# Performance work log

Measured on AMD Instinct MI355X. Metric: run time of the kernel, lower is better.

## Reference

```python
import jax, jax.numpy as jnp
import numpy as np

NUM_HEADS = 16
D_MODEL = 1024
MASK_VALUE = -1000000.0


def setup_inputs() -> dict:
    key = jax.random.key(0)
    ks = jax.random.split(key, 8)
    B, S, D = 2, 2048, D_MODEL
    scale = 1.0 / np.sqrt(D)
    return {
        "queries": jax.random.normal(ks[0], (B, S, D), dtype=jnp.float32),
        "keys": jax.random.normal(ks[1], (B, S, D), dtype=jnp.float32),
        "values": jax.random.normal(ks[2], (B, S, D), dtype=jnp.float32),
        "valid_lens": jax.random.randint(ks[3], (B,), 1, S + 1),
        # Linear weights stored as (in, out); no bias (bias=False)
        "Wq": jax.random.normal(ks[4], (D, D), dtype=jnp.float32) * scale,
        "Wk": jax.random.normal(ks[5], (D, D), dtype=jnp.float32) * scale,
        "Wv": jax.random.normal(ks[6], (D, D), dtype=jnp.float32) * scale,
        "Wo": jax.random.normal(ks[7], (D, D), dtype=jnp.float32) * scale,
    }


def reference(queries, keys, values, valid_lens, Wq, Wk, Wv, Wo):
    B, Sq, D = queries.shape
    Sk = keys.shape[1]
    H = NUM_HEADS
    hd = D // H

    def split_heads(x, S):
        # (B, S, D) -> (B, H, S, hd)
        return x.reshape(B, S, H, hd).transpose(0, 2, 1, 3)

    q = split_heads(queries @ Wq, Sq)
    k = split_heads(keys @ Wk, Sk)
    v = split_heads(values @ Wv, Sk)

    # Faithful to original bug: d_k = queries.size(0) after head-flattening = B*H
    scale = 1.0 / jnp.sqrt(jnp.float32(B * H))
    scores = jnp.einsum("bhqd,bhkd->bhqk", q, k) * scale  # (B,H,Sq,Sk)

    # sequence_mask over last dim, per batch row (valid_lens repeated per head)
    mask = jnp.arange(Sk)[None, None, None, :] < valid_lens[:, None, None, None]
    scores = jnp.where(mask, scores, MASK_VALUE)
    attn = jax.nn.softmax(scores, axis=-1)

    out = jnp.einsum("bhqk,bhkd->bhqd", attn, v)  # (B,H,Sq,hd)
    out = out.transpose(0, 2, 1, 3).reshape(B, Sq, D)
    return out @ Wo
```

## Files before the change

kernel.cpp:

```cpp
#include <hip/hip_runtime.h>
#include <stdint.h>

#define NH 16
#define SEQ 2048
#define DMODEL 1024
#define HD 64
#define NBATCH 2
#define MTOT (NBATCH * SEQ)
#define QSCALE 0.17677669529663687f
#define LOG2E 1.4426950408889634f

typedef __bf16 bf16x8 __attribute__((ext_vector_type(8)));
typedef float f32x4 __attribute__((ext_vector_type(4)));
typedef float f32x16 __attribute__((ext_vector_type(16)));
typedef unsigned uint4v __attribute__((ext_vector_type(4)));

__device__ __forceinline__ unsigned short bf16u(float x) {
  unsigned u = __builtin_bit_cast(unsigned, x);
  u += 0x7fffu + ((u >> 16) & 1u);
  return (unsigned short)(u >> 16);
}

__device__ __forceinline__ float exp2_fast(float x) {
  float r;
  asm("v_exp_f32 %0, %1" : "=v"(r) : "v"(x));
  return r;
}

__device__ __forceinline__ f32x4 mfma16(bf16x8 a, bf16x8 b, f32x4 c) {
  return __builtin_amdgcn_mfma_f32_16x16x32_bf16(a, b, c, 0, 0, 0);
}
__device__ __forceinline__ f32x16 mfma32(bf16x8 a, bf16x8 b, f32x16 c) {
  return __builtin_amdgcn_mfma_f32_32x32x16_bf16(a, b, c, 0, 0, 0);
}

__device__ __forceinline__ void gl16(const void* g, void* l) {
  __builtin_amdgcn_global_load_lds(
      (const __attribute__((address_space(1))) void*)g,
      (__attribute__((address_space(3))) void*)l, 16, 0, 0);
}

__device__ __forceinline__ unsigned cvtpk(float a, float b) {
  unsigned r;
  asm("v_cvt_pk_bf16_f32 %0, %1, %2" : "=v"(r) : "v"(a), "v"(b));
  return r;
}


__global__ __launch_bounds__(256) void prep_kernel(
    const float* __restrict__ x0, const float* __restrict__ x1,
    const float* __restrict__ x2, unsigned short* __restrict__ o0,
    unsigned short* __restrict__ o1, unsigned short* __restrict__ o2,
    const float* __restrict__ w0, const float* __restrict__ w1,
    const float* __restrict__ w2, const float* __restrict__ w3,
    unsigned short* __restrict__ t0, unsigned short* __restrict__ t1,
    unsigned short* __restrict__ t2, unsigned short* __restrict__ t3) {
  const int id = blockIdx.x;
  if (id < 1536) {
    const int src = id >> 9, blk = id & 511;
    const float* s = (src == 0) ? x0 : (src == 1) ? x1 : x2;
    unsigned short* d = (src == 0) ? o0 : (src == 1) ? o1 : o2;
    const int n4 = MTOT * DMODEL / 4;
    for (int i = blk * 256 + threadIdx.x; i < n4; i += 512 * 256) {
      float4 f = reinterpret_cast<const float4*>(s)[i];
      ushort4 u;
      u.x = bf16u(f.x); u.y = bf16u(f.y); u.z = bf16u(f.z); u.w = bf16u(f.w);
      reinterpret_cast<ushort4*>(d)[i] = u;
    }
  } else {
    __shared__ float tile[64][65];
    const int id2 = id - 1536;
    const int wsel = id2 >> 8, tl = id2 & 255;
    const float* w = (wsel == 0) ? w0 : (wsel == 1) ? w1
                     : (wsel == 2) ? w2 : w3;
    unsigned short* t = (wsel == 0) ? t0 : (wsel == 1) ? t1
                        : (wsel == 2) ? t2 : t3;
    const float scl = (wsel == 0) ? QSCALE * LOG2E : 1.0f;
    int n0 = (tl & 15) * 64, k0 = (tl >> 4) * 64;
    int tx = threadIdx.x & 63, ty = threadIdx.x >> 6;
#pragma unroll
    for (int i = 0; i < 16; ++i) {
      int kk = ty * 16 + i;
      tile[kk][tx] = w[(k0 + kk) * DMODEL + n0 + tx];
    }
    __syncthreads();
#pragma unroll
    for (int i = 0; i < 16; ++i) {
      int nn = ty * 16 + i;
      t[(n0 + nn) * DMODEL + k0 + tx] = bf16u(tile[tx][nn] * scl);
    }
  }
}

__global__ __launch_bounds__(256) void gemm_qkv_kernel(
    const unsigned short* __restrict__ xq, const unsigned short* __restrict__ xk,
    const unsigned short* __restrict__ xv,
    const unsigned short* __restrict__ wq, const unsigned short* __restrict__ wk,
    const unsigned short* __restrict__ wv,
    unsigned short* __restrict__ qb, unsigned short* __restrict__ kb,
    unsigned short* __restrict__ vb) {
  __shared__ unsigned short lA[2][128 * 32];
  __shared__ unsigned short lB[2][128 * 32];
  const int z = blockIdx.z;
  const unsigned short* A = (z == 0) ? xq : (z == 1) ? xk : xv;
  const unsigned short* Wt = (z == 0) ? wq : (z == 1) ? wk : wv;
  unsigned short* outb = (z == 0) ? qb : (z == 1) ? kb : vb;

  const int tid = threadIdx.x;
  const int lane = tid & 63, wid = tid >> 6;
  const int wr = wid >> 1, wc = wid & 1;
  const int m0 = blockIdx.x * 128, n0 = blockIdx.y * 128;
  const int lm = lane & 15, lg = lane >> 4;
  const int lk = lg * 8;

  auto stage = [&](int buf, int kt) {
#pragma unroll
    for (int i = 0; i < 2; ++i) {
      int c = tid + i * 256;
      int row = c >> 2, cb = c & 3;
      gl16(A + (m0 + row) * DMODEL + kt * 32 + cb * 8, (char*)lA[buf] + c * 16);
      gl16(Wt + (n0 + row) * DMODEL + kt * 32 + cb * 8, (char*)lB[buf] + c * 16);
    }
  };

  f32x4 acc[4][4] = {};
  stage(0, 0);
  __syncthreads();
  int cur = 0;

  for (int kt = 0; kt < DMODEL / 32; ++kt) {
    if (kt + 1 < DMODEL / 32) stage(cur ^ 1, kt + 1);

    bf16x8 af[4], bfr[4];
#pragma unroll
    for (int x = 0; x < 4; ++x) {
      af[x] = *reinterpret_cast<const bf16x8*>(&lA[cur][(wr * 64 + x * 16 + lm) * 32 + lk]);
      bfr[x] = *reinterpret_cast<const bf16x8*>(&lB[cur][(wc * 64 + x * 16 + lm) * 32 + lk]);
    }
#pragma unroll
    for (int mi = 0; mi < 4; ++mi)
#pragma unroll
      for (int ni = 0; ni < 4; ++ni)
        acc[mi][ni] = mfma16(af[mi], bfr[ni], acc[mi][ni]);

    if (kt + 1 < DMODEL / 32) { __syncthreads(); cur ^= 1; }
  }

#pragma unroll
  for (int mi = 0; mi < 4; ++mi)
#pragma unroll
    for (int ni = 0; ni < 4; ++ni) {
      int col = n0 + wc * 64 + ni * 16 + lm;
#pragma unroll
      for (int r = 0; r < 4; ++r) {
        int row = m0 + wr * 64 + mi * 16 + lg * 4 + r;
        int b = row >> 11, s = row & (SEQ - 1);
        int h = col >> 6, d = col & (HD - 1);
        outb[(((b * NH + h) * SEQ + s) * HD + d)] = bf16u(acc[mi][ni][r]);
      }
    }
}

__global__ __launch_bounds__(256) void gemm_out_kernel(
    const unsigned short* __restrict__ A, const unsigned short* __restrict__ Wt,
    float* __restrict__ outf) {
  __shared__ unsigned short lA[2][128 * 32];
  __shared__ unsigned short lB[2][64 * 32];
  const int tid = threadIdx.x;
  const int lane = tid & 63, wr = tid >> 6;
  const int m0 = blockIdx.x * 128, n0 = blockIdx.y * 64;
  const int lm = lane & 15, lg = lane >> 4;
  const int lk = lg * 8;

  auto stage = [&](int buf, int kt) {
#pragma unroll
    for (int i = 0; i < 2; ++i) {
      int c = tid + i * 256;
      int row = c >> 2, cb = c & 3;
      gl16(A + (m0 + row) * DMODEL + kt * 32 + cb * 8, (char*)lA[buf] + c * 16);
    }
    int c = tid;
    int row = c >> 2, cb = c & 3;
    gl16(Wt + (n0 + row) * DMODEL + kt * 32 + cb * 8, (char*)lB[buf] + c * 16);
  };

  f32x4 acc[2][4] = {};
  stage(0, 0);
  __syncthreads();
  int cur = 0;

  for (int kt = 0; kt < DMODEL / 32; ++kt) {
    if (kt + 1 < DMODEL / 32) stage(cur ^ 1, kt + 1);

    bf16x8 af[2], bfr[4];
#pragma unroll
    for (int x = 0; x < 2; ++x)
      af[x] = *reinterpret_cast<const bf16x8*>(&lA[cur][(wr * 32 + x * 16 + lm) * 32 + lk]);
#pragma unroll
    for (int x = 0; x < 4; ++x)
      bfr[x] = *reinterpret_cast<const bf16x8*>(&lB[cur][(x * 16 + lm) * 32 + lk]);
#pragma unroll
    for (int mi = 0; mi < 2; ++mi)
#pragma unroll
      for (int ni = 0; ni < 4; ++ni)
        acc[mi][ni] = mfma16(af[mi], bfr[ni], acc[mi][ni]);

    if (kt + 1 < DMODEL / 32) { __syncthreads(); cur ^= 1; }
  }

#pragma unroll
  for (int mi = 0; mi < 2; ++mi)
#pragma unroll
    for (int ni = 0; ni < 4; ++ni) {
      int col = n0 + ni * 16 + lm;
#pragma unroll
      for (int r = 0; r < 4; ++r) {
        int row = m0 + wr * 32 + mi * 16 + lg * 4 + r;
        outf[row * DMODEL + col] = acc[mi][ni][r];
      }
    }
}

__global__ __launch_bounds__(256) void attn16_kernel(
    const unsigned short* __restrict__ qb, const unsigned short* __restrict__ kb,
    const unsigned short* __restrict__ vb, const int* __restrict__ vlens,
    unsigned short* __restrict__ ao) {
  __shared__ char klds[4][2][8192];
  const int lane = threadIdx.x & 63;
  const int w = threadIdx.x >> 6;
  const int qi = lane & 31, hi = lane >> 5;
  const int wid = blockIdx.x * 4 + w;
  const int bhi = wid & 31;
  const int chunk = wid >> 5;
  const int b = bhi & 1, h = bhi >> 1;
  const int bh = b * NH + h;
  const int s0w = chunk * 32;
  const int vlen = vlens[b];
  const int nkt = (vlen + 63) >> 6;

  const unsigned short* kbase = kb + bh * SEQ * HD;
  const unsigned short* vbase = vb + (size_t)bh * SEQ * HD;

  const unsigned short* qrow = qb + (bh * SEQ + s0w + qi) * HD;
  bf16x8 qf[4];
#pragma unroll
  for (int ks = 0; ks < 4; ++ks)
    qf[ks] = *reinterpret_cast<const bf16x8*>(qrow + ks * 16 + hi * 8);

  f32x16 oacc[2] = {};
  float m = -3e38f, l = 0.f;

  const int srow = lane >> 3;
  const int scol8 = (lane & 7) ^ (srow & 7);
  auto stageK = [&](int buf, int kt) {
    int k0 = kt * 64;
    char* dst = &klds[w][buf][0];
#pragma unroll
    for (int i = 0; i < 8; ++i)
      gl16(kbase + (size_t)(k0 + i * 8 + srow) * HD + scol8 * 8,
           dst + i * 1024);
  };

  auto readK = [&](bf16x8* kr, int buf) {
    const char* base = &klds[w][buf][0];
#pragma unroll
    for (int kb2 = 0; kb2 < 2; ++kb2)
#pragma unroll
      for (int ks = 0; ks < 4; ++ks) {
        int row = kb2 * 32 + qi;
        int off = row * 128 + ((ks * 32 + hi * 16) ^ ((qi & 7) << 4));
        kr[kb2 * 4 + ks] = *reinterpret_cast<const bf16x8*>(base + off);
      }
  };

  auto body = [&](int t, int buf) {
    const int k0 = t * 64;
    const bool lastt = (t == nkt - 1);

    asm volatile("s_waitcnt vmcnt(0)" ::: "memory");
    __builtin_amdgcn_sched_barrier(0);

    bf16x8 kr[8];
    readK(kr, buf);

    f32x16 s0 = {}, s1 = {};
    __builtin_amdgcn_s_setprio(1);
#pragma unroll
    for (int ks = 0; ks < 4; ++ks) s0 = mfma32(kr[ks], qf[ks], s0);
#pragma unroll
    for (int ks = 0; ks < 4; ++ks) s1 = mfma32(kr[4 + ks], qf[ks], s1);
    __builtin_amdgcn_s_setprio(0);

    bf16x8 vr[8];
#pragma unroll
    for (int db = 0; db < 2; ++db)
#pragma unroll
      for (int f = 0; f < 4; ++f) {
        const unsigned short* vp =
            vbase + (size_t)(k0 + f * 16 + 4 * hi) * HD + db * 32 + qi;
        bf16x8 tv;
#pragma unroll
        for (int j = 0; j < 8; ++j) {
          int koff = ((j & 3) + 8 * (j >> 2)) * HD;
          tv[j] = *reinterpret_cast<const __bf16*>(vp + koff);
        }
        vr[db * 4 + f] = tv;
      }

    if (!lastt) stageK(buf ^ 1, t + 1);

    if (lastt) {
#pragma unroll
      for (int r = 0; r < 16; ++r) {
        int key = k0 + (r & 3) + 8 * (r >> 2) + 4 * hi;
        if (key >= vlen) s0[r] = -1.4426950e6f;
        if (key + 32 >= vlen) s1[r] = -1.4426950e6f;
      }
    }

    float mx8[8];
#pragma unroll
    for (int i = 0; i < 8; ++i)
      mx8[i] = fmaxf(fmaxf(s0[i], s0[i + 8]), fmaxf(s1[i], s1[i + 8]));
#pragma unroll
    for (int st = 4; st; st >>= 1)
#pragma unroll
      for (int i = 0; i < st; ++i) mx8[i] = fmaxf(mx8[i], mx8[i + st]);
    float mx = fmaxf(mx8[0], __shfl_xor(mx8[0], 32, 64));
    float mn = fmaxf(m, mx);
    float sf = exp2_fast(m - mn);
    m = mn;

#pragma unroll
    for (int r = 0; r < 16; ++r) s0[r] = exp2_fast(s0[r] - mn);
#pragma unroll
    for (int r = 0; r < 16; ++r) s1[r] = exp2_fast(s1[r] - mn);
    float sm8[8];
#pragma unroll
    for (int i = 0; i < 8; ++i)
      sm8[i] = (s0[i] + s0[i + 8]) + (s1[i] + s1[i + 8]);
#pragma unroll
    for (int st = 4; st; st >>= 1)
#pragma unroll
      for (int i = 0; i < st; ++i) sm8[i] += sm8[i + st];
    float ps = sm8[0] + __shfl_xor(sm8[0], 32, 64);
    l = l * sf + ps;
#pragma unroll
    for (int db = 0; db < 2; ++db) oacc[db] *= sf;

    bf16x8 pf[4];
    auto packP = [&](const f32x16& s, bf16x8* out) {
#pragma unroll
      for (int f = 0; f < 2; ++f) {
        uint4v wv;
#pragma unroll
        for (int k2 = 0; k2 < 4; ++k2)
          wv[k2] = cvtpk(s[f * 8 + k2 * 2], s[f * 8 + k2 * 2 + 1]);
        out[f] = __builtin_bit_cast(bf16x8, wv);
      }
    };
    packP(s0, pf);
    packP(s1, pf + 2);

    __builtin_amdgcn_s_setprio(1);
#pragma unroll
    for (int db = 0; db < 2; ++db)
#pragma unroll
      for (int f = 0; f < 4; ++f)
        oacc[db] = mfma32(vr[db * 4 + f], pf[f], oacc[db]);
    __builtin_amdgcn_s_setprio(0);
  };

  stageK(0, 0);
  for (int t = 0; t < nkt; ++t) body(t, t & 1);

  const float linv = 1.0f / l;
#pragma unroll
  for (int db = 0; db < 2; ++db)
#pragma unroll
    for (int rq = 0; rq < 4; ++rq) {
      ushort4 o;
      o.x = bf16u(oacc[db][rq * 4 + 0] * linv);
      o.y = bf16u(oacc[db][rq * 4 + 1] * linv);
      o.z = bf16u(oacc[db][rq * 4 + 2] * linv);
      o.w = bf16u(oacc[db][rq * 4 + 3] * linv);
      int d = db * 32 + 8 * rq + 4 * hi;
      *reinterpret_cast<ushort4*>(
          ao + (b * SEQ + s0w + qi) * DMODEL + h * HD + d) = o;
    }
}

extern "C" void kernel_launch(void* const* d_in, const int* in_sizes, int n_in,
                              void* d_out, int out_size, void* d_ws, size_t ws_size,
                              hipStream_t stream) {
  (void)in_sizes; (void)n_in; (void)out_size; (void)ws_size;
  const float* q = (const float*)d_in[0];
  const float* k = (const float*)d_in[1];
  const float* v = (const float*)d_in[2];
  const int* vlens = (const int*)d_in[3];
  const float* Wq = (const float*)d_in[4];
  const float* Wk = (const float*)d_in[5];
  const float* Wv = (const float*)d_in[6];
  const float* Wo = (const float*)d_in[7];
  float* out = (float*)d_out;

  char* ws = (char*)d_ws;
  const size_t MB = 1u << 20;
  unsigned short* xq = (unsigned short*)(ws + 0 * MB);
  unsigned short* xk = (unsigned short*)(ws + 8 * MB);
  unsigned short* xv = (unsigned short*)(ws + 16 * MB);
  unsigned short* wqt = (unsigned short*)(ws + 24 * MB);
  unsigned short* wkt = (unsigned short*)(ws + 26 * MB);
  unsigned short* wvt = (unsigned short*)(ws + 28 * MB);
  unsigned short* wot = (unsigned short*)(ws + 30 * MB);
  unsigned short* qb = (unsigned short*)(ws + 32 * MB);
  unsigned short* kb = (unsigned short*)(ws + 40 * MB);
  unsigned short* vb = (unsigned short*)(ws + 48 * MB);
  unsigned short* ao = (unsigned short*)(ws + 56 * MB);

  prep_kernel<<<dim3(2560), 256, 0, stream>>>(q, k, v, xq, xk, xv,
                                              Wq, Wk, Wv, Wo,
                                              wqt, wkt, wvt, wot);
  gemm_qkv_kernel<<<dim3(32, 8, 3), 256, 0, stream>>>(xq, xk, xv, wqt, wkt, wvt,
                                                      qb, kb, vb);
  attn16_kernel<<<dim3(512), 256, 0, stream>>>(qb, kb, vb, vlens, ao);
  gemm_out_kernel<<<dim3(32, 16), 256, 0, stream>>>(ao, wot, out);
}
```

Baseline: 125.5 us.

## Pre-pack V in MFMA fragment order in QKV GEMM epilogue for vector loads

The QKV GEMM epilogue now writes V into a packed layout that matches the attention kernel's MFMA B-fragment order. Each lane can then load a V fragment with one 16-byte vector load instead of eight scattered 2-byte loads. The K prefetch is moved ahead of the V loads, and launch_bounds now requests 2 blocks per CU. The cost is a scattered, uncoalesced store pattern for V in the GEMM epilogue and possible register pressure from the occupancy hint.

After: 114.3 us. 1.1x faster.

```diff
diff --git a/kernel.cpp b/kernel.cpp
--- a/kernel.cpp
+++ b/kernel.cpp
@@ -98,13 +98,13 @@
     const unsigned short* __restrict__ wq, const unsigned short* __restrict__ wk,
     const unsigned short* __restrict__ wv,
     unsigned short* __restrict__ qb, unsigned short* __restrict__ kb,
-    unsigned short* __restrict__ vb) {
+    unsigned short* __restrict__ vp) {
   __shared__ unsigned short lA[2][128 * 32];
   __shared__ unsigned short lB[2][128 * 32];
   const int z = blockIdx.z;
   const unsigned short* A = (z == 0) ? xq : (z == 1) ? xk : xv;
   const unsigned short* Wt = (z == 0) ? wq : (z == 1) ? wk : wv;
-  unsigned short* outb = (z == 0) ? qb : (z == 1) ? kb : vb;
+  unsigned short* outb = (z == 0) ? qb : (z == 1) ? kb : vp;
 
   const int tid = threadIdx.x;
   const int lane = tid & 63, wid = tid >> 6;
@@ -156,7 +156,19 @@
         int row = m0 + wr * 64 + mi * 16 + lg * 4 + r;
         int b = row >> 11, s = row & (SEQ - 1);
         int h = col >> 6, d = col & (HD - 1);
-        outb[(((b * NH + h) * SEQ + s) * HD + d)] = bf16u(acc[mi][ni][r]);
+        unsigned short val = bf16u(acc[mi][ni][r]);
+        if (z != 2) {
+          outb[(((b * NH + h) * SEQ + s) * HD + d)] = val;
+        } else {
+          int kt2 = s >> 6, rem6 = s & 63;
+          int ff = rem6 >> 4, rem = rem6 & 15;
+          int jj = (rem & 3) | ((rem >> 3) << 2);
+          int hh = (rem >> 2) & 1;
+          size_t pidx =
+              (((((size_t)(b * NH + h) * 32 + kt2) * 2 + (d >> 5)) * 4 + ff) * 64
+               + hh * 32 + (d & 31)) * 8 + jj;
+          outb[pidx] = val;
+        }
       }
     }
 }
@@ -221,9 +233,9 @@
     }
 }
 
-__global__ __launch_bounds__(256) void attn16_kernel(
+__global__ __launch_bounds__(256, 2) void attn17_kernel(
     const unsigned short* __restrict__ qb, const unsigned short* __restrict__ kb,
-    const unsigned short* __restrict__ vb, const int* __restrict__ vlens,
+    const unsigned short* __restrict__ vp, const int* __restrict__ vlens,
     unsigned short* __restrict__ ao) {
   __shared__ char klds[4][2][8192];
   const int lane = threadIdx.x & 63;
@@ -239,7 +251,7 @@
   const int nkt = (vlen + 63) >> 6;
 
   const unsigned short* kbase = kb + bh * SEQ * HD;
-  const unsigned short* vbase = vb + (size_t)bh * SEQ * HD;
+  const unsigned short* vpb = vp + (size_t)bh * 32 * 2 * 4 * 64 * 8;
 
   const unsigned short* qrow = qb + (bh * SEQ + s0w + qi) * HD;
   bf16x8 qf[4];
@@ -291,23 +303,16 @@
     for (int ks = 0; ks < 4; ++ks) s1 = mfma32(kr[4 + ks], qf[ks], s1);
     __builtin_amdgcn_s_setprio(0);
 
+    if (!lastt) stageK(buf ^ 1, t + 1);
+
+    const unsigned short* vtile = vpb + (size_t)t * 2 * 4 * 64 * 8;
     bf16x8 vr[8];
 #pragma unroll
     for (int db = 0; db < 2; ++db)
 #pragma unroll
-      for (int f = 0; f < 4; ++f) {
-        const unsigned short* vp =
-            vbase + (size_t)(k0 + f * 16 + 4 * hi) * HD + db * 32 + qi;
-        bf16x8 tv;
-#pragma unroll
-        for (int j = 0; j < 8; ++j) {
-          int koff = ((j & 3) + 8 * (j >> 2)) * HD;
-          tv[j] = *reinterpret_cast<const __bf16*>(vp + koff);
-        }
-        vr[db * 4 + f] = tv;
-      }
-
-    if (!lastt) stageK(buf ^ 1, t + 1);
+      for (int f = 0; f < 4; ++f)
+        vr[db * 4 + f] = *reinterpret_cast<const bf16x8*>(
+            vtile + ((db * 4 + f) * 64 + lane) * 8);
 
     if (lastt) {
 #pragma unroll
@@ -415,14 +420,14 @@
   unsigned short* wot = (unsigned short*)(ws + 30 * MB);
   unsigned short* qb = (unsigned short*)(ws + 32 * MB);
   unsigned short* kb = (unsigned short*)(ws + 40 * MB);
-  unsigned short* vb = (unsigned short*)(ws + 48 * MB);
+  unsigned short* vpk = (unsigned short*)(ws + 48 * MB);
   unsigned short* ao = (unsigned short*)(ws + 56 * MB);
 
   prep_kernel<<<dim3(2560), 256, 0, stream>>>(q, k, v, xq, xk, xv,
                                               Wq, Wk, Wv, Wo,
                                               wqt, wkt, wvt, wot);
   gemm_qkv_kernel<<<dim3(32, 8, 3), 256, 0, stream>>>(xq, xk, xv, wqt, wkt, wvt,
-                                                      qb, kb, vb);
-  attn16_kernel<<<dim3(512), 256, 0, stream>>>(qb, kb, vb, vlens, ao);
+                                                      qb, kb, vpk);
+  attn17_kernel<<<dim3(512), 256, 0, stream>>>(qb, kb, vpk, vlens, ao);
   gemm_out_kernel<<<dim3(32, 16), 256, 0, stream>>>(ao, wot, out);
 }
```
